# Optimization experiments

Measured on AMD Instinct MI355X. Metric: run time of the kernel, lower is better.

## Reference

```python
import jax, jax.numpy as jnp
import numpy as np

B, S, F, D = 2, 576, 16, 512   # batch, spatial tokens (24x24), frames, query_dim
H, C = 8, 64                   # heads, dim_head; inner = H*C = 512


def setup_inputs() -> dict:
    key = jax.random.key(0)
    ks = jax.random.split(key, 6)
    x = jax.random.normal(ks[0], (B, S, F, D), jnp.float32)
    # alternating drop pattern over frames 2..F-1; identical per batch row,
    # as the module requires (it reshapes kept indices to [bs, -1] and takes
    # valid_num from row 0)
    pat = jnp.tile(jnp.array([1, 0], jnp.int64), (F - 2) // 2)
    drop_mask = jnp.broadcast_to(pat, (B, F - 2))
    sd = 1.0 / np.sqrt(D)
    Wq = jax.random.normal(ks[1], (D, H * C), jnp.float32) * sd
    Wk = jax.random.normal(ks[2], (D, H * C), jnp.float32) * sd
    Wv = jax.random.normal(ks[3], (D, H * C), jnp.float32) * sd
    Wout = jax.random.normal(ks[4], (H * C, D), jnp.float32) * (1.0 / np.sqrt(H * C))
    bout = jnp.zeros((D,), jnp.float32)
    return {"x": x, "drop_mask": drop_mask, "Wq": Wq, "Wk": Wk, "Wv": Wv,
            "Wout": Wout, "bout": bout}


def _sdpa(q, k, v):
    # q: [..., Lq, C], k/v: [..., Lk, C]; xformers default scale = 1/sqrt(C)
    scale = 1.0 / np.sqrt(q.shape[-1])
    logits = jnp.einsum('...qc,...kc->...qk', q, k) * scale
    w = jax.nn.softmax(logits, axis=-1)
    return jnp.einsum('...qk,...kc->...qc', w, v)


def reference(x, drop_mask, Wq, Wk, Wv, Wout, bout):
    b, s, f, _ = x.shape
    h, c = H, C
    q = x @ Wq  # [b, s, f, h*c]
    k = x @ Wk
    v = x @ Wv

    # ---- per-frame spatial self-attention for frames 1: ('b s f (h c) -> (b f h) s c')
    def to_bfhsc(t, nf):
        return t.reshape(b, s, nf, h, c).transpose(0, 2, 3, 1, 4)  # b f h s c

    ress = _sdpa(to_bfhsc(q[:, :, 1:], f - 1),
                 to_bfhsc(k[:, :, 1:], f - 1),
                 to_bfhsc(v[:, :, 1:], f - 1))            # [b, f-1, h, s, c]
    ress = ress.transpose(0, 3, 1, 2, 4).reshape(b, s, f - 1, h * c)

    # ---- frame-0 temporal attention over first 2 frames + non-dropped frames
    dm = np.asarray(drop_mask)
    valid = int((f - 2) - dm[0].sum())
    # kept frame indices (into frames 2..f-1), per batch row
    kept = np.stack([np.nonzero(dm[i] == 0)[0] for i in range(b)])  # [b, valid]
    idx = jnp.asarray(kept)[:, None, :, None]
    ka, va = k[:, :, 2:], v[:, :, 2:]                     # [b, s, f-2, h*c]
    ki = jnp.take_along_axis(ka, jnp.broadcast_to(idx, (b, s, valid, h * c)), axis=2)
    vi = jnp.take_along_axis(va, jnp.broadcast_to(idx, (b, s, valid, h * c)), axis=2)
    dk = jnp.concatenate([k[:, :, :2], ki], axis=2)        # [b, s, df, h*c]
    dv = jnp.concatenate([v[:, :, :2], vi], axis=2)
    df = 2 + valid

    qt = q[:, :, 0].reshape(b, s, h, c).transpose(0, 2, 1, 3)  # [b, h, s, c]
    kt = dk.reshape(b, s, df, h, c).transpose(0, 3, 1, 2, 4).reshape(b, h, s * df, c)
    vt = dv.reshape(b, s, df, h, c).transpose(0, 3, 1, 2, 4).reshape(b, h, s * df, c)
    resq = _sdpa(qt, kt, vt)                               # [b, h, s, c]
    resq = resq.transpose(0, 2, 1, 3).reshape(b, s, 1, h * c)

    res = jnp.concatenate([resq, ress], axis=2)            # [b, s, f, h*c]
    return res @ Wout + bout                               # [b, s, f, D]
```

## Files before the change

kernel.cpp:

```cpp
#include <hip/hip_runtime.h>
#include <math.h>

#define Bb 2
#define Ss 576
#define Ff 16
#define Hh 8
#define Cc 64
#define HC 512
#define Mrows (Bb * Ss * Ff)

typedef __bf16 bf16x8 __attribute__((ext_vector_type(8)));
typedef float  f32x4  __attribute__((ext_vector_type(4)));
typedef float  f32x16 __attribute__((ext_vector_type(16)));
typedef unsigned short u16;
typedef unsigned int   u32;

#if __has_builtin(__builtin_amdgcn_exp2f)
#define EXP2(x) __builtin_amdgcn_exp2f(x)
#else
#define EXP2(x) exp2f(x)
#endif

#define QSCALE 0.18033688011112042f

__device__ __forceinline__ u16 f2bf(float f) {
    union { __bf16 b; u16 u; } cv;
    cv.b = (__bf16)f;
    return cv.u;
}

__device__ __forceinline__ f32x16 zero16() {
    f32x16 z;
#pragma unroll
    for (int i = 0; i < 16; ++i) z[i] = 0.f;
    return z;
}

__device__ __forceinline__ int swz8(int row, int g) {
    return row * 64 + (((g ^ (row & 7) ^ (((row >> 3) & 1) << 1)) & 7) << 3);
}
__device__ __forceinline__ int swzg(int row, int g) {
    return row * 32 + (((g ^ (row & 3)) & 3) << 3);
}

__device__ __forceinline__ uint4 pack8(float4 a, float4 b) {
    union { u16 s[8]; uint4 v; } u;
    u.s[0] = f2bf(a.x); u.s[1] = f2bf(a.y); u.s[2] = f2bf(a.z); u.s[3] = f2bf(a.w);
    u.s[4] = f2bf(b.x); u.s[5] = f2bf(b.y); u.s[6] = f2bf(b.z); u.s[7] = f2bf(b.w);
    return u.v;
}

__global__ __launch_bounds__(256) void convert_w_kernel(
    const float* __restrict__ W0, const float* __restrict__ W1,
    const float* __restrict__ W2, const float* __restrict__ W3,
    u16* __restrict__ Wt)
{
    __shared__ float Ts[64][65];
    const int mz = blockIdx.z;
    const float* W = (mz == 0) ? W0 : (mz == 1) ? W1 : (mz == 2) ? W2 : W3;
    u16* Wo = Wt + (size_t)mz * 512 * 512;
    const int k0 = blockIdx.x * 64, n0 = blockIdx.y * 64;
    const int t = threadIdx.x;
#pragma unroll
    for (int p = 0; p < 4; ++p) {
        int idx = t + p * 256;
        int row = idx >> 4, cg = idx & 15;
        *(float4*)&Ts[row][cg * 4] =
            *(const float4*)&W[(size_t)(k0 + row) * 512 + n0 + cg * 4];
    }
    __syncthreads();
#pragma unroll
    for (int p = 0; p < 2; ++p) {
        int idx = t + p * 256;
        int row = idx >> 3, cg = idx & 7;
        union { u16 s[8]; uint4 v; } u;
#pragma unroll
        for (int j = 0; j < 8; ++j) u.s[j] = f2bf(Ts[cg * 8 + j][row]);
        *(uint4*)&Wo[(size_t)(n0 + row) * 512 + k0 + cg * 8] = u.v;
    }
}

__global__ __launch_bounds__(256) void qkv_kernel(
    const float* __restrict__ x, const u16* __restrict__ Wt,
    u16* __restrict__ q, u16* __restrict__ k, u16* __restrict__ vT)
{
    __shared__ u16 As[128 * 32];
    __shared__ u16 Bs[128 * 32];
    const int bi = blockIdx.x;
    const int mt = bi % 144;
    const int mm = bi / 144;
    const int nt = mm & 3, mat = mm >> 2;
    const int t = threadIdx.x;
    const int w = t >> 6, L = t & 63;
    const int m0 = mt * 128, n0 = nt * 128;
    const int wm = (w >> 1) * 64, wn = (w & 1) * 64;

    const int srow = t >> 2, scg = t & 3;
    const int ma0 = m0 + srow, ma1 = m0 + srow + 64;
    const int b0 = ma0 / 9216, r0 = ma0 % 9216, f0 = r0 / 576, s0 = r0 % 576;
    const int b1 = ma1 / 9216, r1 = ma1 % 9216, f1 = r1 / 576, s1 = r1 % 576;
    const float* xp0 = x + ((size_t)(b0 * 576 + s0) * 16 + f0) * 512 + scg * 8;
    const float* xp1 = x + ((size_t)(b1 * 576 + s1) * 16 + f1) * 512 + scg * 8;
    const u16* Bp = Wt + (size_t)mat * 512 * 512 + (size_t)(n0 + srow) * 512 + scg * 8;
    const int lo0 = swzg(srow, scg), lo1 = swzg(srow + 64, scg);

    float4 fa0 = *(const float4*)xp0, fa0b = *(const float4*)(xp0 + 4);
    float4 fa1 = *(const float4*)xp1, fa1b = *(const float4*)(xp1 + 4);
    uint4 ub0 = *(const uint4*)Bp;
    uint4 ub1 = *(const uint4*)(Bp + 64 * 512);

    f32x4 acc[4][4];
#pragma unroll
    for (int i = 0; i < 4; ++i)
#pragma unroll
        for (int j = 0; j < 4; ++j) acc[i][j] = (f32x4){0.f, 0.f, 0.f, 0.f};

    for (int k0 = 0; k0 < 512; k0 += 32) {
        __syncthreads();
        *(uint4*)&As[lo0] = pack8(fa0, fa0b);
        *(uint4*)&As[lo1] = pack8(fa1, fa1b);
        *(uint4*)&Bs[lo0] = ub0;
        *(uint4*)&Bs[lo1] = ub1;
        __syncthreads();
        if (k0 < 480) {
            fa0  = *(const float4*)(xp0 + k0 + 32);
            fa0b = *(const float4*)(xp0 + k0 + 36);
            fa1  = *(const float4*)(xp1 + k0 + 32);
            fa1b = *(const float4*)(xp1 + k0 + 36);
            ub0  = *(const uint4*)(Bp + k0 + 32);
            ub1  = *(const uint4*)(Bp + k0 + 32 + 64 * 512);
        }
        bf16x8 af[4], bfr[4];
#pragma unroll
        for (int i = 0; i < 4; ++i) {
            af[i]  = *(const bf16x8*)&As[swzg(wm + 16 * i + (L & 15), L >> 4)];
            bfr[i] = *(const bf16x8*)&Bs[swzg(wn + 16 * i + (L & 15), L >> 4)];
        }
#pragma unroll
        for (int i = 0; i < 4; ++i)
#pragma unroll
            for (int j = 0; j < 4; ++j)
                acc[i][j] = __builtin_amdgcn_mfma_f32_16x16x32_bf16(
                    af[i], bfr[j], acc[i][j], 0, 0, 0);
    }

    if (mat < 2) {
        u16* Cout = (mat == 0) ? q : k;
        const float scale = (mat == 0) ? QSCALE : 1.0f;
#pragma unroll
        for (int i = 0; i < 4; ++i)
#pragma unroll
            for (int j = 0; j < 4; ++j)
#pragma unroll
                for (int r = 0; r < 4; ++r) {
                    int row = m0 + wm + 16 * i + (L >> 4) * 4 + r;
                    int col = n0 + wn + 16 * j + (L & 15);
                    float vv = acc[i][j][r] * scale;
                    float pvv = __shfl_xor(vv, 1);
                    if (!(L & 1)) {
                        u32 pk2 = (u32)f2bf(vv) | ((u32)f2bf(pvv) << 16);
                        *(u32*)(Cout + (size_t)row * 512 + col) = pk2;
                    }
                }
    } else {
#pragma unroll
        for (int i = 0; i < 4; ++i) {
            int row = m0 + wm + 16 * i + (L >> 4) * 4;
            int bb = row / 9216, rr = row % 9216;
            int f = rr / 576, s = rr % 576;
#pragma unroll
            for (int j = 0; j < 4; ++j) {
                int col = n0 + wn + 16 * j + (L & 15);
                int h = col >> 6, c = col & 63;
                union { u16 s4[4]; uint2 v; } u;
#pragma unroll
                for (int r = 0; r < 4; ++r) u.s4[r] = f2bf(acc[i][j][r]);
                *(uint2*)&vT[((((size_t)(bb * 16 + f) * 8 + h) * 64 + c) * 576) + s] = u.v;
            }
        }
    }
}

__global__ __launch_bounds__(256) void gemm_out_kernel(
    const u16* __restrict__ res, const u16* __restrict__ Wt3,
    const float* __restrict__ bout, float* __restrict__ out)
{
    __shared__ u16 As[128 * 32];
    __shared__ u16 Bs[128 * 32];
    const int bi = blockIdx.x;
    const int mt = bi % 144, nt = bi / 144;
    const int t = threadIdx.x;
    const int w = t >> 6, L = t & 63;
    const int m0 = mt * 128, n0 = nt * 128;
    const int wm = (w >> 1) * 64, wn = (w & 1) * 64;

    const int srow = t >> 2, scg = t & 3;
    const u16* Ap = res + (size_t)(m0 + srow) * 512 + scg * 8;
    const u16* Bp = Wt3 + (size_t)(n0 + srow) * 512 + scg * 8;
    const int lo0 = swzg(srow, scg), lo1 = swzg(srow + 64, scg);

    uint4 ua0 = *(const uint4*)Ap;
    uint4 ua1 = *(const uint4*)(Ap + 64 * 512);
    uint4 ub0 = *(const uint4*)Bp;
    uint4 ub1 = *(const uint4*)(Bp + 64 * 512);

    f32x4 acc[4][4];
#pragma unroll
    for (int i = 0; i < 4; ++i)
#pragma unroll
        for (int j = 0; j < 4; ++j) acc[i][j] = (f32x4){0.f, 0.f, 0.f, 0.f};

    for (int k0 = 0; k0 < 512; k0 += 32) {
        __syncthreads();
        *(uint4*)&As[lo0] = ua0;
        *(uint4*)&As[lo1] = ua1;
        *(uint4*)&Bs[lo0] = ub0;
        *(uint4*)&Bs[lo1] = ub1;
        __syncthreads();
        if (k0 < 480) {
            ua0 = *(const uint4*)(Ap + k0 + 32);
            ua1 = *(const uint4*)(Ap + k0 + 32 + 64 * 512);
            ub0 = *(const uint4*)(Bp + k0 + 32);
            ub1 = *(const uint4*)(Bp + k0 + 32 + 64 * 512);
        }
        bf16x8 af[4], bfr[4];
#pragma unroll
        for (int i = 0; i < 4; ++i) {
            af[i]  = *(const bf16x8*)&As[swzg(wm + 16 * i + (L & 15), L >> 4)];
            bfr[i] = *(const bf16x8*)&Bs[swzg(wn + 16 * i + (L & 15), L >> 4)];
        }
#pragma unroll
        for (int i = 0; i < 4; ++i)
#pragma unroll
            for (int j = 0; j < 4; ++j)
                acc[i][j] = __builtin_amdgcn_mfma_f32_16x16x32_bf16(
                    af[i], bfr[j], acc[i][j], 0, 0, 0);
    }

#pragma unroll
    for (int i = 0; i < 4; ++i)
#pragma unroll
        for (int r = 0; r < 4; ++r) {
            int row = m0 + wm + 16 * i + (L >> 4) * 4 + r;
            int bb = row / 9216, rr = row % 9216;
            int f = rr / 576, s = rr % 576;
            size_t obase = ((size_t)(bb * 576 + s) * 16 + f) * 512;
#pragma unroll
            for (int j = 0; j < 4; ++j) {
                int col = n0 + wn + 16 * j + (L & 15);
                out[obase + col] = acc[i][j][r] + bout[col];
            }
        }
}

__global__ __launch_bounds__(256, 4) void attn_kernel(
    const u16* __restrict__ q, const u16* __restrict__ k,
    const u16* __restrict__ vT, const int* __restrict__ dm,
    u16* __restrict__ res, float* __restrict__ po, float* __restrict__ pl)
{
    __shared__ u16 Ks[64 * 64];
    __shared__ u16 Vts[64 * 64];
    __shared__ u16 Ps[128 * 64];
    __shared__ int fl[16];

    const int t = threadIdx.x;
    const int w = t >> 6, L = t & 63;
    const int half = L >> 5, l31 = L & 31;
    const int bi = blockIdx.x;

    int b, h, qt, qframe, fi, mode;
    if (bi < 720) {
        mode = 0;
        qt = bi / 144;
        int g = bi % 144;
        int bh = g / 9; fi = g % 9;
        b = bh >> 3; h = bh & 7; qframe = 0;
    } else {
        mode = 1;
        int u = bi - 720;
        int g = u % 240;
        qt = u / 240;
        b = g / 120;
        int rr = g % 120;
        qframe = 1 + (rr >> 3); h = rr & 7; fi = 0;
    }

    if (t == 0) {
        int n = 0;
        fl[n++] = 0; fl[n++] = 1;
        for (int j = 0; j < Ff - 2; ++j)
            if (dm[b * (Ff - 2) + j] == 0) fl[n++] = 2 + j;
    }
    __syncthreads();

    const int kf = (mode == 0) ? fl[fi] : qframe;

    const int q0 = qt * 128;
    const bool active = (q0 + 32 * w) < Ss;
    const int qrow = q0 + 32 * w + l31;
    const int prow = 32 * w + l31;

    bf16x8 qf[4];
    if (active) {
        const u16* qp = q + ((size_t)(b * 16 + qframe) * Ss + qrow) * 512 + h * 64 + 8 * half;
#pragma unroll
        for (int ks = 0; ks < 4; ++ks) qf[ks] = *(const bf16x8*)(qp + 16 * ks);
    }

    float lsum = 0.f;
    f32x16 o[2] = {zero16(), zero16()};

    const int srow = t >> 2, sc2 = (t & 3) * 2;
    const int lk0 = swz8(srow, sc2), lk1 = swz8(srow, sc2 + 1);
    const u16* kbase = k + ((size_t)(b * 16 + kf) * Ss) * 512 + h * 64;
    const u16* vbase = vT + (((size_t)(b * 16 + kf) * 8 + h) * 64) * (size_t)Ss;

    uint4 ka, kb2, va, vb2;
    {
        const u16* kp = kbase + (size_t)srow * 512 + sc2 * 8;
        ka  = *(const uint4*)kp;
        kb2 = *(const uint4*)(kp + 8);
        const u16* vp = vbase + (size_t)srow * Ss + sc2 * 8;
        va  = *(const uint4*)vp;
        vb2 = *(const uint4*)(vp + 8);
    }

    for (int kt = 0; kt < 9; ++kt) {
        __syncthreads();
        *(uint4*)&Ks[lk0]  = ka;
        *(uint4*)&Ks[lk1]  = kb2;
        *(uint4*)&Vts[lk0] = va;
        *(uint4*)&Vts[lk1] = vb2;
        __syncthreads();

        if (kt < 8) {
            int s0 = (kt + 1) * 64;
            const u16* kp = kbase + (size_t)(s0 + srow) * 512 + sc2 * 8;
            ka  = *(const uint4*)kp;
            kb2 = *(const uint4*)(kp + 8);
            const u16* vp = vbase + (size_t)srow * Ss + s0 + sc2 * 8;
            va  = *(const uint4*)vp;
            vb2 = *(const uint4*)(vp + 8);
        }

        if (active) {
            f32x16 st[2] = {zero16(), zero16()};
#pragma unroll
            for (int ks = 0; ks < 4; ++ks) {
                bf16x8 a0 = *(const bf16x8*)&Ks[swz8(l31,      2 * ks + half)];
                bf16x8 a1 = *(const bf16x8*)&Ks[swz8(32 + l31, 2 * ks + half)];
                st[0] = __builtin_amdgcn_mfma_f32_32x32x16_bf16(a0, qf[ks], st[0], 0, 0, 0);
                st[1] = __builtin_amdgcn_mfma_f32_32x32x16_bf16(a1, qf[ks], st[1], 0, 0, 0);
            }
            const int rsw = (prow & 7) ^ (((prow >> 3) & 1) << 1);
#pragma unroll
            for (int mg = 0; mg < 2; ++mg)
#pragma unroll
                for (int g = 0; g < 4; ++g) {
                    float p0 = EXP2(st[mg][4 * g + 0]);
                    float p1 = EXP2(st[mg][4 * g + 1]);
                    float p2 = EXP2(st[mg][4 * g + 2]);
                    float p3 = EXP2(st[mg][4 * g + 3]);
                    lsum += (p0 + p1) + (p2 + p3);
                    union { u16 s4[4]; uint2 v; } u;
                    u.s4[0] = f2bf(p0); u.s4[1] = f2bf(p1);
                    u.s4[2] = f2bf(p2); u.s4[3] = f2bf(p3);
                    int ch = 4 * mg + g;
                    *(uint2*)&Ps[prow * 64 + (((ch ^ rsw) & 7) << 3) + half * 4] = u.v;
                }
#pragma unroll
            for (int ks = 0; ks < 4; ++ks) {
                bf16x8 pb = *(const bf16x8*)&Ps[swz8(prow, 2 * ks + half)];
                bf16x8 v0 = *(const bf16x8*)&Vts[swz8(l31,      2 * ks + half)];
                bf16x8 v1 = *(const bf16x8*)&Vts[swz8(32 + l31, 2 * ks + half)];
                o[0] = __builtin_amdgcn_mfma_f32_32x32x16_bf16(v0, pb, o[0], 0, 0, 0);
                o[1] = __builtin_amdgcn_mfma_f32_32x32x16_bf16(v1, pb, o[1], 0, 0, 0);
            }
        }
    }

    if (!active) return;
    lsum += __shfl_xor(lsum, 32);

    if (mode == 1) {
        float inv = 1.f / lsum;
        u16* rp = res + ((size_t)(b * 16 + qframe) * Ss + qrow) * 512 + h * 64;
#pragma unroll
        for (int cg = 0; cg < 2; ++cg)
#pragma unroll
            for (int g = 0; g < 4; ++g) {
                union { u16 s4[4]; uint2 v; } u;
#pragma unroll
                for (int r = 0; r < 4; ++r) u.s4[r] = f2bf(o[cg][4 * g + r] * inv);
                *(uint2*)&rp[32 * cg + 8 * g + 4 * half] = u.v;
            }
    } else {
        int bh = b * 8 + h;
        float* pp = po + ((size_t)(fi * 16 + bh) * Ss + qrow) * 64;
#pragma unroll
        for (int cg = 0; cg < 2; ++cg)
#pragma unroll
            for (int g = 0; g < 4; ++g) {
                float4 v4 = make_float4(o[cg][4 * g + 0], o[cg][4 * g + 1],
                                        o[cg][4 * g + 2], o[cg][4 * g + 3]);
                *(float4*)&pp[32 * cg + 8 * g + 4 * half] = v4;
            }
        if (half == 0) pl[(size_t)(fi * 16 + bh) * Ss + qrow] = lsum;
    }
}

__global__ __launch_bounds__(256) void merge_kernel(
    const float* __restrict__ po, const float* __restrict__ pl,
    u16* __restrict__ res)
{
    int tid = blockIdx.x * 256 + threadIdx.x;
    int c4 = tid & 15;
    int rem = tid >> 4;
    int qg = rem % Ss;
    int bh = rem / Ss;
    int b = bh >> 3, h = bh & 7;
    float4 acc = make_float4(0.f, 0.f, 0.f, 0.f);
    float ls = 0.f;
#pragma unroll
    for (int fi = 0; fi < 9; ++fi) {
        const float4 v = *(const float4*)&po[((size_t)(fi * 16 + bh) * Ss + qg) * 64 + c4 * 4];
        acc.x += v.x; acc.y += v.y; acc.z += v.z; acc.w += v.w;
        ls += pl[(size_t)(fi * 16 + bh) * Ss + qg];
    }
    float inv = 1.f / ls;
    union { u16 s4[4]; uint2 v; } u;
    u.s4[0] = f2bf(acc.x * inv); u.s4[1] = f2bf(acc.y * inv);
    u.s4[2] = f2bf(acc.z * inv); u.s4[3] = f2bf(acc.w * inv);
    *(uint2*)&res[((size_t)(b * 16 + 0) * Ss + qg) * 512 + h * 64 + c4 * 4] = u.v;
}

extern "C" void kernel_launch(void* const* d_in, const int* in_sizes, int n_in,
                              void* d_out, int out_size, void* d_ws, size_t ws_size,
                              hipStream_t stream)
{
    (void)in_sizes; (void)n_in; (void)out_size; (void)ws_size;
    const float* x    = (const float*)d_in[0];
    const int*   dmsk = (const int*)  d_in[1];
    const float* Wq   = (const float*)d_in[2];
    const float* Wk   = (const float*)d_in[3];
    const float* Wv   = (const float*)d_in[4];
    const float* Wout = (const float*)d_in[5];
    const float* bout = (const float*)d_in[6];
    float* out = (float*)d_out;

    const size_t NE = (size_t)Mrows * HC;
    u16* q   = (u16*)d_ws;
    u16* kk  = q   + NE;
    u16* vT  = kk  + NE;
    u16* res = vT  + NE;
    u16* Wt  = res + NE;
    float* po = (float*)(Wt + (size_t)4 * 512 * 512);
    float* pl = po + (size_t)9 * 16 * Ss * 64;

    convert_w_kernel<<<dim3(8, 8, 4), 256, 0, stream>>>(Wq, Wk, Wv, Wout, Wt);
    qkv_kernel<<<1728, 256, 0, stream>>>(x, Wt, q, kk, vT);
    attn_kernel<<<1920, 256, 0, stream>>>(q, kk, vT, dmsk, res, po, pl);
    merge_kernel<<<576, 256, 0, stream>>>(po, pl, res);
    gemm_out_kernel<<<576, 256, 0, stream>>>(
        res, Wt + (size_t)3 * 512 * 512, bout, out);
}
```

Measured before the change: 239.8 us.

## Keep softmax probabilities in registers via permlane32 swap instead of LDS round-trip

The P tile in the attention kernel is no longer written to shared memory and read back as an MFMA operand. Its layout is rebuilt in registers with permlane32_swap, so the S and PV MFMAs are interleaved per 32-key half. The frame-index table built by thread 0 (with its __syncthreads) is replaced by each thread scanning the drop mask itself. This removes LDS traffic, frees LDS space for occupancy and drops one barrier, but depends on the permlane register layout exactly matching the old Ps layout.

```diff
diff --git a/kernel.cpp b/kernel.cpp
--- a/kernel.cpp
+++ b/kernel.cpp
@@ -260,8 +260,6 @@
 {
     __shared__ u16 Ks[64 * 64];
     __shared__ u16 Vts[64 * 64];
-    __shared__ u16 Ps[128 * 64];
-    __shared__ int fl[16];
 
     const int t = threadIdx.x;
     const int w = t >> 6, L = t & 63;
@@ -285,20 +283,22 @@
         qframe = 1 + (rr >> 3); h = rr & 7; fi = 0;
     }
 
-    if (t == 0) {
-        int n = 0;
-        fl[n++] = 0; fl[n++] = 1;
-        for (int j = 0; j < Ff - 2; ++j)
-            if (dm[b * (Ff - 2) + j] == 0) fl[n++] = 2 + j;
-    }
-    __syncthreads();
-
-    const int kf = (mode == 0) ? fl[fi] : qframe;
+    int kf;
+    if (mode == 1) {
+        kf = qframe;
+    } else if (fi < 2) {
+        kf = fi;
+    } else {
+        int n = 2; kf = 2;
+#pragma unroll
+        for (int j = 0; j < Ff - 2; ++j) {
+            if (dm[b * (Ff - 2) + j] == 0) { if (n == fi) kf = 2 + j; ++n; }
+        }
+    }
 
     const int q0 = qt * 128;
     const bool active = (q0 + 32 * w) < Ss;
     const int qrow = q0 + 32 * w + l31;
-    const int prow = 32 * w + l31;
 
     bf16x8 qf[4];
     if (active) {
@@ -344,37 +344,35 @@
         }
 
         if (active) {
-            f32x16 st[2] = {zero16(), zero16()};
-#pragma unroll
-            for (int ks = 0; ks < 4; ++ks) {
-                bf16x8 a0 = *(const bf16x8*)&Ks[swz8(l31,      2 * ks + half)];
-                bf16x8 a1 = *(const bf16x8*)&Ks[swz8(32 + l31, 2 * ks + half)];
-                st[0] = __builtin_amdgcn_mfma_f32_32x32x16_bf16(a0, qf[ks], st[0], 0, 0, 0);
-                st[1] = __builtin_amdgcn_mfma_f32_32x32x16_bf16(a1, qf[ks], st[1], 0, 0, 0);
-            }
-            const int rsw = (prow & 7) ^ (((prow >> 3) & 1) << 1);
-#pragma unroll
-            for (int mg = 0; mg < 2; ++mg)
-#pragma unroll
-                for (int g = 0; g < 4; ++g) {
-                    float p0 = EXP2(st[mg][4 * g + 0]);
-                    float p1 = EXP2(st[mg][4 * g + 1]);
-                    float p2 = EXP2(st[mg][4 * g + 2]);
-                    float p3 = EXP2(st[mg][4 * g + 3]);
-                    lsum += (p0 + p1) + (p2 + p3);
-                    union { u16 s4[4]; uint2 v; } u;
-                    u.s4[0] = f2bf(p0); u.s4[1] = f2bf(p1);
-                    u.s4[2] = f2bf(p2); u.s4[3] = f2bf(p3);
-                    int ch = 4 * mg + g;
-                    *(uint2*)&Ps[prow * 64 + (((ch ^ rsw) & 7) << 3) + half * 4] = u.v;
+#pragma unroll
+            for (int hb = 0; hb < 2; ++hb) {
+                f32x16 st = zero16();
+#pragma unroll
+                for (int ks = 0; ks < 4; ++ks) {
+                    bf16x8 a = *(const bf16x8*)&Ks[swz8(32 * hb + l31, 2 * ks + half)];
+                    st = __builtin_amdgcn_mfma_f32_32x32x16_bf16(a, qf[ks], st, 0, 0, 0);
                 }
 #pragma unroll
-            for (int ks = 0; ks < 4; ++ks) {
-                bf16x8 pb = *(const bf16x8*)&Ps[swz8(prow, 2 * ks + half)];
-                bf16x8 v0 = *(const bf16x8*)&Vts[swz8(l31,      2 * ks + half)];
-                bf16x8 v1 = *(const bf16x8*)&Vts[swz8(32 + l31, 2 * ks + half)];
-                o[0] = __builtin_amdgcn_mfma_f32_32x32x16_bf16(v0, pb, o[0], 0, 0, 0);
-                o[1] = __builtin_amdgcn_mfma_f32_32x32x16_bf16(v1, pb, o[1], 0, 0, 0);
+                for (int kk = 0; kk < 2; ++kk) {
+                    const int ks = 2 * hb + kk;
+                    float e0 = EXP2(st[8 * kk + 0]), e1 = EXP2(st[8 * kk + 1]);
+                    float e2 = EXP2(st[8 * kk + 2]), e3 = EXP2(st[8 * kk + 3]);
+                    float e4 = EXP2(st[8 * kk + 4]), e5 = EXP2(st[8 * kk + 5]);
+                    float e6 = EXP2(st[8 * kk + 6]), e7 = EXP2(st[8 * kk + 7]);
+                    lsum += ((e0 + e1) + (e2 + e3)) + ((e4 + e5) + (e6 + e7));
+                    u32 x0 = (u32)f2bf(e0) | ((u32)f2bf(e1) << 16);
+                    u32 z0 = (u32)f2bf(e2) | ((u32)f2bf(e3) << 16);
+                    u32 x1 = (u32)f2bf(e4) | ((u32)f2bf(e5) << 16);
+                    u32 z1 = (u32)f2bf(e6) | ((u32)f2bf(e7) << 16);
+                    auto sx = __builtin_amdgcn_permlane32_swap(x0, x1, false, false);
+                    auto sz = __builtin_amdgcn_permlane32_swap(z0, z1, false, false);
+                    union { u32 u[4]; bf16x8 v; } pu;
+                    pu.u[0] = sx[0]; pu.u[1] = sz[0]; pu.u[2] = sx[1]; pu.u[3] = sz[1];
+                    bf16x8 v0 = *(const bf16x8*)&Vts[swz8(l31,      2 * ks + half)];
+                    bf16x8 v1 = *(const bf16x8*)&Vts[swz8(32 + l31, 2 * ks + half)];
+                    o[0] = __builtin_amdgcn_mfma_f32_32x32x16_bf16(v0, pu.v, o[0], 0, 0, 0);
+                    o[1] = __builtin_amdgcn_mfma_f32_32x32x16_bf16(v1, pu.v, o[1], 0, 0, 0);
+                }
             }
         }
     }
```

Measured after the change: 229.7 us. 1.04x faster.
